# Kernel optimization log

Measured on AMD Instinct MI355X. Metric: run time of the kernel, lower is better.

Reference implementation:

```python
import jax, jax.numpy as jnp
import numpy as np

B, S, T = 32, 64, 64
D = 512          # model_size == controller hidden == cell_size
R = 4            # read heads
M = 64           # nr_cells
V = 10000        # vocab
IF = R * D + 3 * D + 5 * R + 3   # DNC interface vector size (3607)
NN_IN = D + R * D                # controller input: x + read vectors
CLIP = 20.0
EPS = 1e-6


def _cosine(mem, keys):
    # mem (B,m,w), keys (B,h,w) -> (B,h,m) batched cosine similarity
    mn = mem / (jnp.linalg.norm(mem, axis=2, keepdims=True) + EPS)
    kn = keys / (jnp.linalg.norm(keys, axis=2, keepdims=True) + EPS)
    return jnp.einsum('bhw,bmw->bhm', kn, mn)


def _allocate(usage):
    # usage (B,m) -> allocation weights (B,1,m)
    u = EPS + (1.0 - EPS) * usage
    phi = jnp.argsort(u, axis=1)                      # ascending: least used first
    su = jnp.take_along_axis(u, phi, axis=1)
    excl = jnp.cumprod(jnp.concatenate([jnp.ones_like(su[:, :1]), su[:, :-1]], axis=1), axis=1)
    sa = (1.0 - su) * excl
    return jnp.take_along_axis(sa, jnp.argsort(phi, axis=1), axis=1)[:, None, :]


def _memory_step(xi, st):
    memory, link, prec, rw, ww, usage = st
    b = xi.shape[0]
    # --- parse interface vector (same slicing as dnc.Memory, independent_linears=False) ---
    rk = jnp.tanh(xi[:, :R * D].reshape(b, R, D))                        # read keys
    rs = jax.nn.softplus(xi[:, R * D:R * D + R])                         # read strengths
    wk = jnp.tanh(xi[:, R * D + R:R * D + R + D].reshape(b, 1, D))       # write key
    ws = jax.nn.softplus(xi[:, R * D + R + D])[:, None]                  # write strength
    er = jax.nn.sigmoid(xi[:, R * D + R + D + 1:R * D + R + 2 * D + 1].reshape(b, 1, D))
    wv = jnp.tanh(xi[:, R * D + R + 2 * D + 1:R * D + R + 3 * D + 1].reshape(b, 1, D))
    fg = jax.nn.sigmoid(xi[:, R * D + R + 3 * D + 1:R * D + 2 * R + 3 * D + 1])   # free gates
    ag = jax.nn.sigmoid(xi[:, R * D + 2 * R + 3 * D + 1])[:, None, None]          # alloc gate
    wg = jax.nn.sigmoid(xi[:, R * D + 2 * R + 3 * D + 2])[:, None, None]          # write gate
    modes = jax.nn.softmax(xi[:, R * D + 2 * R + 3 * D + 3:R * D + 5 * R + 3 * D + 3].reshape(b, R, 3), axis=2)
    # --- write ---
    usage = usage + (1 - usage) * (1 - jnp.prod(1 - ww, axis=1))
    usage = usage * jnp.prod(1 - fg[:, :, None] * rw, axis=1)
    wcw = jax.nn.softmax(_cosine(memory, wk) * ws[:, :, None], axis=2)   # (B,1,M)
    alloc = _allocate(usage)
    ww = wg * (ag * alloc + (1 - ag) * wcw)                              # (B,1,M)
    reset = jnp.prod(1 - ww[:, :, :, None] * er[:, :, None, :], axis=1)  # (B,M,D)
    memory = memory * reset + jnp.einsum('bhm,bhw->bmw', ww, wv)
    ww_i, ww_j = ww[:, :, :, None], ww[:, :, None, :]
    link = (1 - ww_i - ww_j) * link + ww_i * prec[:, :, None, :]
    link = link * (1 - jnp.eye(M, dtype=link.dtype))                     # zero diagonal
    prec = (1 - jnp.sum(ww, axis=2, keepdims=True)) * prec + ww
    # --- read ---
    cw = jax.nn.softmax(_cosine(memory, rk) * rs[:, :, None], axis=2)    # (B,R,M)
    l0 = link[:, 0]
    fwd = jnp.einsum('bnm,brm->brn', l0, rw)
    bwd = jnp.einsum('bmn,brm->brn', l0, rw)
    rw = modes[:, :, 0:1] * bwd + modes[:, :, 1:2] * fwd + modes[:, :, 2:3] * cw
    rv = jnp.einsum('brm,bmw->brw', rw, memory)                          # read vectors
    return (memory, link, prec, rw, ww, usage), rv


def _lstm_cell(x, h, c, Wih, Whh, bih, bhh):
    g = x @ Wih.T + bih + h @ Whh.T + bhh
    i, f, gg, o = jnp.split(g, 4, axis=-1)
    c2 = jax.nn.sigmoid(f) * c + jax.nn.sigmoid(i) * jnp.tanh(gg)
    return jax.nn.sigmoid(o) * jnp.tanh(c2), c2


def _dnc_run(x, p, mem0):
    # x: (B,L,D). Faithful to ixaxaar dnc.py: each timestep input is concat(x_t, initial last_read=zeros).
    b, L, _ = x.shape
    xin = jnp.concatenate([x, jnp.zeros((b, L, R * D), x.dtype)], axis=-1)
    h = jnp.zeros((2, b, D), x.dtype)
    c = jnp.zeros((2, b, D), x.dtype)

    def step(carry, x_t):
        (h, c), mem = carry
        h0, c0 = _lstm_cell(x_t, h[0], c[0], p['Wih0'], p['Whh0'], p['bih0'], p['bhh0'])
        h1, c1 = _lstm_cell(h0, h[1], c[1], p['Wih1'], p['Whh1'], p['bih1'], p['bhh1'])
        out = jnp.clip(h1, -CLIP, CLIP)
        xi = out @ p['Wi'].T + p['bi']
        mem, rv = _memory_step(xi, mem)
        full = jnp.concatenate([out, rv.reshape(b, R * D)], axis=-1)
        y = full @ p['Wo'].T + p['bo']
        return ((jnp.stack([h0, h1]), jnp.stack([c0, c1])), mem), y

    (_, memT), ys = jax.lax.scan(step, ((h, c), mem0), jnp.swapaxes(xin, 0, 1))
    return jnp.swapaxes(ys, 0, 1), memT


def _init_mem(b, dtype):
    return (jnp.zeros((b, M, D), dtype), jnp.zeros((b, 1, M, M), dtype),
            jnp.zeros((b, 1, M), dtype), jnp.zeros((b, R, M), dtype),
            jnp.zeros((b, 1, M), dtype), jnp.zeros((b, M), dtype))


_PNAMES = ['Wih0', 'Whh0', 'bih0', 'bhh0', 'Wih1', 'Whh1', 'bih1', 'bhh1', 'Wi', 'bi', 'Wo', 'bo']


def setup_inputs() -> dict:
    key = jax.random.key(0)
    ks = iter(jax.random.split(key, 40))

    def p(shape, s=0.05):
        return jax.random.normal(next(ks), shape, dtype=jnp.float32) * s

    d = {'emb_src': p((V, D), 0.5), 'emb_tgt': p((V, D), 0.5)}
    shapes = [(4 * D, NN_IN), (4 * D, D), (4 * D,), (4 * D,), (4 * D, D), (4 * D, D), (4 * D,), (4 * D,),
              (IF, D), (IF,), (D, NN_IN), (D,)]
    for pre in ('enc', 'dec'):
        for n, sh in zip(_PNAMES, shapes):
            d[pre + '_' + n] = p(sh)
    d['fc_W'] = p((V, D))
    d['fc_b'] = p((V,))
    d['input'] = jax.random.randint(next(ks), (B, S), 0, V, dtype=jnp.int32)
    d['tgt'] = jax.random.randint(next(ks), (B, T), 0, V, dtype=jnp.int32)
    return d


def reference(emb_src, emb_tgt,
              enc_Wih0, enc_Whh0, enc_bih0, enc_bhh0, enc_Wih1, enc_Whh1, enc_bih1, enc_bhh1,
              enc_Wi, enc_bi, enc_Wo, enc_bo,
              dec_Wih0, dec_Whh0, dec_bih0, dec_bhh0, dec_Wih1, dec_Whh1, dec_bih1, dec_bhh1,
              dec_Wi, dec_bi, dec_Wo, dec_bo,
              fc_W, fc_b, input, tgt):
    enc_vals = [enc_Wih0, enc_Whh0, enc_bih0, enc_bhh0, enc_Wih1, enc_Whh1, enc_bih1, enc_bhh1,
                enc_Wi, enc_bi, enc_Wo, enc_bo]
    dec_vals = [dec_Wih0, dec_Whh0, dec_bih0, dec_bhh0, dec_Wih1, dec_Whh1, dec_bih1, dec_bhh1,
                dec_Wi, dec_bi, dec_Wo, dec_bo]
    enc_p = dict(zip(_PNAMES, enc_vals))
    dec_p = dict(zip(_PNAMES, dec_vals))
    src = emb_src[input]                                   # (B,S,D)
    _, mem = _dnc_run(src, enc_p, _init_mem(src.shape[0], src.dtype))
    out, _ = _dnc_run(emb_tgt[tgt], dec_p, mem)            # decoder reuses encoder memory state
    logits = out @ fc_W.T + fc_b                           # (B,T,V)
    return jnp.transpose(logits, (0, 2, 1))                # (B,V,T)
```

## Files before the change

### kernel.cpp

```cpp
#include <hip/hip_runtime.h>

#define BB   32
#define DD   512
#define RR   4
#define MM   64
#define VV   10000
#define TT   64
#define IFX  3607
#define NNIN 2560
#define EPSF 1e-6f

typedef unsigned short u16;

__device__ __forceinline__ float bf(u16 u){ return __uint_as_float(((unsigned)u)<<16); }
__device__ __forceinline__ float4 b4f(ushort4 u){
  float4 f; f.x = bf(u.x); f.y = bf(u.y); f.z = bf(u.z); f.w = bf(u.w); return f;
}
__device__ __forceinline__ u16 f2b(float f){
  unsigned u = __float_as_uint(f);
  u += 0x7fffu + ((u>>16)&1u);
  return (u16)(u>>16);
}
__device__ __forceinline__ float sigmf(float x){ return 1.f/(1.f+__expf(-x)); }
__device__ __forceinline__ float softplusf(float x){ return x > 20.f ? x : log1pf(__expf(x)); }
__device__ __forceinline__ float wredSum(float v){
  #pragma unroll
  for (int s=1;s<64;s<<=1) v += __shfl_xor(v,s,64);
  return v;
}
__device__ __forceinline__ float wredMax(float v){
  #pragma unroll
  for (int s=1;s<64;s<<=1) v = fmaxf(v, __shfl_xor(v,s,64));
  return v;
}

__device__ __forceinline__ float ldg_c(const float* p){
  return __hip_atomic_load(const_cast<float*>(p), __ATOMIC_RELAXED, __HIP_MEMORY_SCOPE_AGENT);
}
__device__ __forceinline__ void stg_c(float* p, float v){
  __hip_atomic_store(p, v, __ATOMIC_RELAXED, __HIP_MEMORY_SCOPE_AGENT);
}
__device__ __forceinline__ unsigned ldg_cu(const unsigned* p){
  return __hip_atomic_load(const_cast<unsigned*>(p), __ATOMIC_RELAXED, __HIP_MEMORY_SCOPE_AGENT);
}
__device__ __forceinline__ void stg_cu(unsigned* p, unsigned v){
  __hip_atomic_store(p, v, __ATOMIC_RELAXED, __HIP_MEMORY_SCOPE_AGENT);
}

__device__ __forceinline__ void ldg_cv4x2(const float* p0,const float* p1, float4& a,float4& b){
  asm volatile("global_load_dwordx4 %0, %2, off sc0 sc1\n\t"
               "global_load_dwordx4 %1, %3, off sc0 sc1\n\t"
               "s_waitcnt vmcnt(0)"
               : "=&v"(a),"=&v"(b)
               : "v"(p0),"v"(p1)
               : "memory");
}
__device__ __forceinline__ void ldg_c4s(const float* p0,const float* p1,const float* p2,const float* p3,
                                        float& a,float& b,float& c,float& d){
  asm volatile("global_load_dword %0, %4, off sc0 sc1\n\t"
               "global_load_dword %1, %5, off sc0 sc1\n\t"
               "global_load_dword %2, %6, off sc0 sc1\n\t"
               "global_load_dword %3, %7, off sc0 sc1\n\t"
               "s_waitcnt vmcnt(0)"
               : "=&v"(a),"=&v"(b),"=&v"(c),"=&v"(d)
               : "v"(p0),"v"(p1),"v"(p2),"v"(p3)
               : "memory");
}
__device__ __forceinline__ void ldg_c2s(const float* p0,const float* p1, float& a,float& b){
  asm volatile("global_load_dword %0, %2, off sc0 sc1\n\t"
               "global_load_dword %1, %3, off sc0 sc1\n\t"
               "s_waitcnt vmcnt(0)"
               : "=&v"(a),"=&v"(b)
               : "v"(p0),"v"(p1)
               : "memory");
}

#define SM_FLOATS 9600
#define NBLK 256u
#define NTHR 512

__device__ __forceinline__ void gbar5(unsigned* flags, unsigned* gen, unsigned ep){
  asm volatile("s_waitcnt vmcnt(0) lgkmcnt(0)" ::: "memory");
  __syncthreads();
  if (threadIdx.x == 0) stg_cu(&flags[blockIdx.x*16], ep);
  if (blockIdx.x == 0) {
    if (threadIdx.x < 256) {
      const unsigned* f = &flags[threadIdx.x*16];
      while (ldg_cu(f) < ep) __builtin_amdgcn_s_sleep(1);
    }
    __syncthreads();
    if (threadIdx.x == 0) stg_cu(gen, ep);
  } else if (threadIdx.x == 0) {
    while (ldg_cu(gen) < ep) __builtin_amdgcn_s_sleep(1);
  }
  __syncthreads();
}

#define LW_OFF 5312
#define XW_OFF 4224

__device__ __forceinline__ void preload_lstm(float* S, int tile,
    const float* __restrict__ Wx, int wx_stride, const float* __restrict__ Wh)
{
  float* WL = S + LW_OFF;
  const int tid = threadIdx.x;
  const int dblk = tile*8;
  for (int i = tid; i < 8192; i += NTHR) {
    const int r  = i >> 8;
    const int k4 = (i & 255) * 4;
    const int gr = ((r>>3)<<9) + dblk + (r&7);
    float4 v;
    if (k4 < 512) v = *(const float4*)&Wx[(size_t)gr*wx_stride + k4];
    else          v = *(const float4*)&Wh[(size_t)gr*512 + (k4-512)];
    *(float4*)&WL[r*1028 + k4] = v;
  }
}

__device__ __forceinline__ void preload_xi(float* S, int xtile, const float* __restrict__ Wi){
  float* XW = S + XW_OFF;
  const int tid = threadIdx.x;
  for (int i = tid; i < 8192; i += NTHR) {
    const int r  = i >> 7;
    const int k4 = (i & 127) * 4;
    int cr = xtile*64 + r; if (cr >= IFX) cr = IFX-1;
    *(float4*)&XW[r*516 + k4] = *(const float4*)&Wi[(size_t)cr*512 + k4];
  }
}

__device__ __noinline__ void lstm_tile_p(
    float* S, int tile,
    const float* __restrict__ bx, const float* __restrict__ bh,
    const float* emb, const int* seq, int t,
    const float* xf,
    const float* hprev, float* hcur,
    float* cst, float* outc, u16* full)
{
  float (*As)[132] = (float(*)[132])S;
  int* idxs = (int*)(S + 5280);
  const float* WL = S + LW_OFF;
  const int tid = threadIdx.x;
  const int w  = tid >> 6;
  const int bg = (tid >> 3) & 7;
  const int ks = tid & 7;
  const int dblk = tile * 8;
  const int ba = tid >> 5;
  const int bbs = ba + 16;
  const int f0 = (tid & 31) * 4;
  float acc[4][4];
  #pragma unroll
  for (int i=0;i<4;i++)
    #pragma unroll
    for (int j=0;j<4;j++) acc[i][j]=0.f;
  if (emb != nullptr && tid < 32) idxs[tid] = seq[tid*64 + t];
  __syncthreads();
  #define LSRC(ch, bb_) ( ((ch) < 4) \
      ? ((emb != nullptr) ? &emb[(size_t)idxs[bb_]*512 + (ch)*128 + f0] \
                          : &xf[(bb_)*512 + (ch)*128 + f0]) \
      : &hprev[(bb_)*512 + ((ch)*128 - 512) + f0] )
  for (int chunk = 0; chunk < 8; ++chunk) {
    {
      float4 v0, v1;
      ldg_cv4x2(LSRC(chunk,ba), LSRC(chunk,bbs), v0, v1);
      *(float4*)&As[ba][f0]  = v0;
      *(float4*)&As[bbs][f0] = v1;
    }
    __syncthreads();
    const int kb = chunk*128;
    #pragma unroll
    for (int m = 0; m < 4; ++m) {
      const int kk = ks*4 + m*32;
      float4 w4[4], a4[4];
      #pragma unroll
      for (int j=0;j<4;j++) w4[j] = *(const float4*)&WL[(w + 8*j)*1028 + kb + kk];
      #pragma unroll
      for (int i=0;i<4;i++) a4[i] = *(const float4*)&As[bg + 8*i][kk];
      #pragma unroll
      for (int i=0;i<4;i++)
        #pragma unroll
        for (int j=0;j<4;j++)
          acc[i][j] = fmaf(a4[i].x,w4[j].x, fmaf(a4[i].y,w4[j].y,
                      fmaf(a4[i].z,w4[j].z, fmaf(a4[i].w,w4[j].w, acc[i][j]))));
    }
    __syncthreads();
  }
  #undef LSRC
  #pragma unroll
  for (int i=0;i<4;i++)
    #pragma unroll
    for (int j=0;j<4;j++){
      float v = acc[i][j];
      v += __shfl_xor(v,1,64);
      v += __shfl_xor(v,2,64);
      v += __shfl_xor(v,4,64);
      acc[i][j] = v;
    }
  if (ks == 0) {
    const int d = dblk + w;
    float bias[4];
    #pragma unroll
    for (int j=0;j<4;j++){
      const int gcol = (j<<9) + d;
      bias[j] = bx[gcol] + bh[gcol];
    }
    #pragma unroll
    for (int i=0;i<4;i++){
      const int b = bg + 8*i;
      const int cid = b*512 + d;
      const float gi = acc[i][0] + bias[0];
      const float gf = acc[i][1] + bias[1];
      const float gg = acc[i][2] + bias[2];
      const float go = acc[i][3] + bias[3];
      const float cv = sigmf(gf)*cst[cid] + sigmf(gi)*tanhf(gg);
      const float hv = sigmf(go)*tanhf(cv);
      cst[cid] = cv;
      stg_c(&hcur[cid], hv);
      if (outc != nullptr) {
        const float oc = fminf(fmaxf(hv,-20.f),20.f);
        stg_c(&outc[cid], oc);
        if (full != nullptr) full[((size_t)t*32 + b)*2560 + d] = f2b(oc);
      }
    }
  }
  __syncthreads();
}

__device__ __noinline__ void xi_tile_p(
    float* S, int xtile,
    const float* outc, const float* __restrict__ bi, float* xi)
{
  float (*As)[132] = (float(*)[132])S;
  const float* XW = S + XW_OFF;
  const int tid = threadIdx.x;
  const int w  = tid >> 6;
  const int l  = tid & 63;
  const int tt = l >> 2;
  const int ks = l & 3;
  const int cg = 2*w + (tt>>3);
  const int bg = tt & 7;
  const int ba = tid >> 5;
  const int bbs = ba + 16;
  const int f0 = (tid & 31) * 4;
  float acc[4][4];
  #pragma unroll
  for (int i=0;i<4;i++)
    #pragma unroll
    for (int j=0;j<4;j++) acc[i][j]=0.f;
  for (int chunk = 0; chunk < 4; ++chunk) {
    {
      const int kb0 = chunk*128;
      float4 v0, v1;
      ldg_cv4x2(&outc[ba*512 + kb0 + f0], &outc[bbs*512 + kb0 + f0], v0, v1);
      *(float4*)&As[ba][f0]  = v0;
      *(float4*)&As[bbs][f0] = v1;
    }
    __syncthreads();
    const int kb = chunk*128;
    #pragma unroll
    for (int m = 0; m < 8; ++m) {
      const int kk = ks*4 + m*16;
      float4 w4[4], a4[4];
      #pragma unroll
      for (int j=0;j<4;j++) w4[j] = *(const float4*)&XW[(cg + 16*j)*516 + kb + kk];
      #pragma unroll
      for (int i=0;i<4;i++) a4[i] = *(const float4*)&As[bg + 8*i][kk];
      #pragma unroll
      for (int i=0;i<4;i++)
        #pragma unroll
        for (int j=0;j<4;j++)
          acc[i][j] = fmaf(a4[i].x,w4[j].x, fmaf(a4[i].y,w4[j].y,
                      fmaf(a4[i].z,w4[j].z, fmaf(a4[i].w,w4[j].w, acc[i][j]))));
    }
    __syncthreads();
  }
  #pragma unroll
  for (int i=0;i<4;i++)
    #pragma unroll
    for (int j=0;j<4;j++){
      float v = acc[i][j];
      v += __shfl_xor(v,1,64);
      v += __shfl_xor(v,2,64);
      acc[i][j] = v;
    }
  if (ks == 0) {
    #pragma unroll
    for (int j=0;j<4;j++){
      const int col = xtile*64 + cg + 16*j;
      if (col < IFX) {
        const float bias = bi[col];
        #pragma unroll
        for (int i=0;i<4;i++)
          stg_c(&xi[(size_t)(bg + 8*i)*IFX + col], acc[i][j] + bias);
      }
    }
  }
  __syncthreads();
}

__device__ __constant__ int kSidx[23] = {
  2048,2049,2050,2051, 2564, 3589,3590,3591,3592, 3593, 3594,
  3595,3596,3597, 3598,3599,3600, 3601,3602,3603, 3604,3605,3606
};

#define MEMPITCH 516
#define L_MEM   0
#define L_LINK  33024
#define L_RK    37184
#define L_WK    39232
#define L_RWP   39744
#define L_PREC  40000
#define L_USAGE 40064
#define L_WCW   40128
#define L_U     40192
#define L_WW    40256
#define L_CWA   40320
#define L_SC    40576
#define L_SRAW  40616
#define L_END   40640
#define DYN_LDS_BYTES 162560

__device__ __noinline__ void mem_tile_lds(
    float* S, int b, const float* xi, u16* full, int t)
{
  const int tid = threadIdx.x;
  const float* xb = xi + (size_t)b*IFX;
  float* MEMS = S + L_MEM;
  float* LNK  = S + L_LINK;
  float (*rk_s)[512] = (float(*)[512])(S + L_RK);
  float* wk_s  = S + L_WK;
  float* RWP   = S + L_RWP;
  float* PREC  = S + L_PREC;
  float* USAGE = S + L_USAGE;
  float* wcw_s = S + L_WCW;
  float* u_s   = S + L_U;
  float* WW    = S + L_WW;
  float* sorted_s = S + L_CWA;
  float* excl_s   = S + L_CWA + 64;
  int*   rank_s   = (int*)(S + L_CWA + 128);
  float (*cw_s)[64] = (float(*)[64])(S + L_CWA);
  float* sc   = S + L_SC;
  float* sraw = S + L_SRAW;

  {
    const float* base = xb + tid*4;
    float v0,v1,v2,v3;
    ldg_c4s(base+0,base+1,base+2,base+3, v0,v1,v2,v3);
    float* d = &rk_s[tid>>7][(tid&127)*4];
    d[0]=tanhf(v0); d[1]=tanhf(v1); d[2]=tanhf(v2); d[3]=tanhf(v3);
  }
  if (tid < 128) {
    const float* base = xb + 2052 + tid*4;
    float v0,v1,v2,v3;
    ldg_c4s(base+0,base+1,base+2,base+3, v0,v1,v2,v3);
    float* d = &wk_s[tid*4];
    d[0]=tanhf(v0); d[1]=tanhf(v1); d[2]=tanhf(v2); d[3]=tanhf(v3);
  }
  if (tid < 23) sraw[tid] = ldg_c(&xb[kSidx[tid]]);
  __syncthreads();
  if (tid == 0) {
    for (int r=0;r<4;r++) sc[r] = softplusf(sraw[r]);
    sc[4] = softplusf(sraw[4]);
    for (int r=0;r<4;r++) sc[5+r] = sigmf(sraw[5+r]);
    sc[9]  = sigmf(sraw[9]);
    sc[10] = sigmf(sraw[10]);
    for (int r=0;r<4;r++) {
      const float a0=sraw[11+3*r], a1=sraw[12+3*r], a2=sraw[13+3*r];
      const float mx=fmaxf(a0,fmaxf(a1,a2));
      const float e0=__expf(a0-mx), e1=__expf(a1-mx), e2=__expf(a2-mx);
      const float s=e0+e1+e2;
      sc[11+3*r]=e0/s; sc[12+3*r]=e1/s; sc[13+3*r]=e2/s;
    }
  }
  if (tid < 256) {
    const int wid = tid>>6, ln = tid&63;
    float p = 0.f;
    for (int i = ln; i < 512; i += 64) { const float v = rk_s[wid][i]; p = fmaf(v,v,p); }
    p = wredSum(p);
    if (ln == 0) sc[24+wid] = sqrtf(p);
    if (wid == 1) {
      float q2 = 0.f;
      for (int i = ln; i < 512; i += 64) { const float v = wk_s[i]; q2 = fmaf(v,v,q2); }
      q2 = wredSum(q2);
      if (ln == 0) sc[23] = sqrtf(q2);
    }
  }
  __syncthreads();
  if (tid < 256) {
    const int m = tid>>2, q = tid&3;
    const float* mr = MEMS + m*MEMPITCH;
    float d = 0.f, ss = 0.f;
    for (int i = q*128; i < q*128+128; i += 4) {
      const float4 mv = *(const float4*)&mr[i];
      d = fmaf(mv.x, wk_s[i  ], d); d = fmaf(mv.y, wk_s[i+1], d);
      d = fmaf(mv.z, wk_s[i+2], d); d = fmaf(mv.w, wk_s[i+3], d);
      ss = fmaf(mv.x,mv.x,ss); ss = fmaf(mv.y,mv.y,ss);
      ss = fmaf(mv.z,mv.z,ss); ss = fmaf(mv.w,mv.w,ss);
    }
    d  += __shfl_xor(d,1,64);  d  += __shfl_xor(d,2,64);
    ss += __shfl_xor(ss,1,64); ss += __shfl_xor(ss,2,64);
    if (q == 0) wcw_s[m] = d / ((sqrtf(ss)+EPSF)*(sc[23]+EPSF)) * sc[4];
  }
  if (tid < 64) {
    const float uo = USAGE[tid];
    float u = uo + (1.f-uo)*WW[tid];
    #pragma unroll
    for (int r=0;r<4;r++) u *= (1.f - sc[5+r]*RWP[r*64+tid]);
    USAGE[tid] = u;
  }
  __syncthreads();
  if (tid < 64) {
    const float v = wcw_s[tid];
    const float mx = wredMax(v);
    const float e = __expf(v-mx);
    const float s2 = wredSum(e);
    wcw_s[tid] = e/s2;
    u_s[tid] = EPSF + (1.f-EPSF)*USAGE[tid];
  }
  __syncthreads();
  if (tid < 64) {
    const float u = u_s[tid]; int rk2 = 0;
    for (int j=0;j<64;j++){ const float uj = u_s[j]; rk2 += (uj<u) || (uj==u && j<tid); }
    rank_s[tid] = rk2; sorted_s[rk2] = u;
  }
  __syncthreads();
  if (tid == 0) { float run = 1.f; for (int p2=0;p2<64;p2++){ excl_s[p2]=run; run*=sorted_s[p2]; } }
  __syncthreads();
  if (tid < 64) {
    const float al = (1.f - u_s[tid]) * excl_s[rank_s[tid]];
    const float wwv = sc[10]*(sc[9]*al + (1.f-sc[9])*wcw_s[tid]);
    WW[tid] = wwv;
    const float s3 = wredSum(wwv);
    if (tid==0) sc[28] = s3;
  }
  __syncthreads();
  {
    float e0,w0;
    ldg_c2s(&xb[2565+tid], &xb[3077+tid], e0, w0);
    const float er0 = sigmf(e0);
    const float wv0 = tanhf(w0);
    #pragma unroll 4
    for (int m=0;m<64;m++){
      const float wwm = WW[m];
      float* p = MEMS + m*MEMPITCH + tid;
      p[0] = p[0]*(1.f - wwm*er0) + wwm*wv0;
    }
  }
  __syncthreads();
  for (int e = tid; e < 4096; e += NTHR) {
    const int i2 = e>>6, j2 = e&63;
    const float lv = LNK[i2*65+j2];
    LNK[i2*65+j2] = (i2==j2) ? 0.f
               : ((1.f - WW[i2] - WW[j2])*lv + WW[i2]*PREC[j2]);
  }
  __syncthreads();
  if (tid < 64) PREC[tid] = (1.f - sc[28])*PREC[tid] + WW[tid];
  __syncthreads();
  const int r6 = tid>>6, m6 = tid&63;
  if (tid < 256) {
    const float* mr = MEMS + m6*MEMPITCH;
    const float* rkr = rk_s[r6];
    float d = 0.f, ss = 0.f;
    for (int i=0;i<512;i+=4){
      const float4 mv = *(const float4*)&mr[i];
      d = fmaf(mv.x, rkr[i  ], d); d = fmaf(mv.y, rkr[i+1], d);
      d = fmaf(mv.z, rkr[i+2], d); d = fmaf(mv.w, rkr[i+3], d);
      ss = fmaf(mv.x,mv.x,ss); ss = fmaf(mv.y,mv.y,ss);
      ss = fmaf(mv.z,mv.z,ss); ss = fmaf(mv.w,mv.w,ss);
    }
    const float cv = d / ((sqrtf(ss)+EPSF)*(sc[24+r6]+EPSF)) * sc[r6];
    const float mx = wredMax(cv);
    const float e = __expf(cv-mx);
    const float s2 = wredSum(e);
    cw_s[r6][m6] = e/s2;
  }
  __syncthreads();
  float rn = 0.f;
  if (tid < 256) {
    float fw = 0.f, bw = 0.f;
    #pragma unroll 8
    for (int m3=0;m3<64;m3++){
      const float rp = RWP[r6*64+m3];
      fw = fmaf(LNK[m6*65+m3], rp, fw);
      bw = fmaf(LNK[m3*65+m6], rp, bw);
    }
    rn = sc[11+3*r6]*bw + sc[12+3*r6]*fw + sc[13+3*r6]*cw_s[r6][m6];
  }
  __syncthreads();
  if (tid < 256) RWP[r6*64+m6] = rn;
  __syncthreads();
  if (full != nullptr && tid < 256) {
    const int l = tid&63, r8 = tid>>6;
    float a[8];
    #pragma unroll
    for (int j=0;j<8;j++) a[j]=0.f;
    for (int m3=0;m3<64;m3++){
      const float rv_ = RWP[r8*64+m3];
      const float* mr = MEMS + m3*MEMPITCH + 2*l;
      #pragma unroll
      for (int j=0;j<4;j++){
        const float2 v = *(const float2*)&mr[128*j];
        a[2*j]   = fmaf(rv_, v.x, a[2*j]);
        a[2*j+1] = fmaf(rv_, v.y, a[2*j+1]);
      }
    }
    u16* dst = full + ((size_t)t*32 + b)*2560 + 512 + r8*512;
    #pragma unroll
    for (int j=0;j<4;j++){
      const unsigned wd = (unsigned)f2b(a[2*j]) | ((unsigned)f2b(a[2*j+1])<<16);
      *(unsigned*)&dst[2*l + 128*j] = wd;
    }
  }
  __syncthreads();
}

__device__ __noinline__ void lstm_tile_g(
    float* sm, int tile,
    const float* __restrict__ Wx, int wx_stride,
    const float* __restrict__ Wh,
    const float* __restrict__ bx, const float* __restrict__ bh,
    const float* emb, const int* seq, int t,
    const float* xf,
    const float* hprev, float* hcur,
    float* cst, float* outc, u16* full)
{
  float (*As)[132] = (float(*)[132])sm;
  float (*Ws)[132] = (float(*)[132])(sm + 4224);
  float* gs = sm + 8448;
  int* idxs = (int*)(sm + 9504);
  const int tid = threadIdx.x;
  const int c = tid & 31;
  const int dblk = tile * 8;
  const int gcol = ((c>>3)<<9) + dblk + (c&7);
  const int b0 = (tid >> 5) * 4;
  float acc0=0.f, acc1=0.f, acc2=0.f, acc3=0.f;
  if (emb != nullptr && tid < 32) idxs[tid] = seq[tid*64 + t];
  __syncthreads();
  for (int chunk = 0; chunk < 8; ++chunk) {
    const int k0 = chunk * 128;
    const bool xp = (chunk < 4);
    for (int i = tid; i < 1024; i += 256) {
      const int bb2 = i >> 5, f4i = (i & 31)*4;
      if (xp && emb != nullptr) {
        *(float4*)&As[bb2][f4i] = *(const float4*)&emb[(size_t)idxs[bb2]*512 + k0 + f4i];
      } else {
        const float* src = xp ? &xf[bb2*512 + k0 + f4i]
                              : &hprev[bb2*512 + (k0-512) + f4i];
        As[bb2][f4i+0] = ldg_c(src+0);
        As[bb2][f4i+1] = ldg_c(src+1);
        As[bb2][f4i+2] = ldg_c(src+2);
        As[bb2][f4i+3] = ldg_c(src+3);
      }
    }
    for (int i = tid; i < 1024; i += 256) {
      const int r = i >> 5, f4i = (i & 31)*4;
      const int gr = ((r>>3)<<9) + dblk + (r&7);
      const float4 v = xp ? *(const float4*)&Wx[(size_t)gr*wx_stride + k0 + f4i]
                          : *(const float4*)&Wh[(size_t)gr*512 + (k0-512) + f4i];
      *(float4*)&Ws[r][f4i] = v;
    }
    __syncthreads();
    #pragma unroll 8
    for (int kk = 0; kk < 128; kk += 4) {
      const float4 w4 = *(const float4*)&Ws[c][kk];
      const float4 a0 = *(const float4*)&As[b0+0][kk];
      const float4 a1 = *(const float4*)&As[b0+1][kk];
      const float4 a2 = *(const float4*)&As[b0+2][kk];
      const float4 a3 = *(const float4*)&As[b0+3][kk];
      acc0 = fmaf(a0.x,w4.x,fmaf(a0.y,w4.y,fmaf(a0.z,w4.z,fmaf(a0.w,w4.w,acc0))));
      acc1 = fmaf(a1.x,w4.x,fmaf(a1.y,w4.y,fmaf(a1.z,w4.z,fmaf(a1.w,w4.w,acc1))));
      acc2 = fmaf(a2.x,w4.x,fmaf(a2.y,w4.y,fmaf(a2.z,w4.z,fmaf(a2.w,w4.w,acc2))));
      acc3 = fmaf(a3.x,w4.x,fmaf(a3.y,w4.y,fmaf(a3.z,w4.z,fmaf(a3.w,w4.w,acc3))));
    }
    __syncthreads();
  }
  const float bias = bx[gcol] + bh[gcol];
  gs[c*33 + b0+0] = acc0 + bias;
  gs[c*33 + b0+1] = acc1 + bias;
  gs[c*33 + b0+2] = acc2 + bias;
  gs[c*33 + b0+3] = acc3 + bias;
  __syncthreads();
  {
    const int b2 = tid & 31, dl2 = tid >> 5;
    const float gi = gs[(0*8+dl2)*33 + b2];
    const float gf = gs[(1*8+dl2)*33 + b2];
    const float gg = gs[(2*8+dl2)*33 + b2];
    const float go = gs[(3*8+dl2)*33 + b2];
    const int d = dblk + dl2;
    const int cid = b2*512 + d;
    const float cv = sigmf(gf)*cst[cid] + sigmf(gi)*tanhf(gg);
    const float hv = sigmf(go)*tanhf(cv);
    cst[cid] = cv;
    stg_c(&hcur[cid], hv);
    if (outc != nullptr) {
      const float oc = fminf(fmaxf(hv,-20.f),20.f);
      stg_c(&outc[cid], oc);
      if (full != nullptr) full[((size_t)t*32 + b2)*2560 + d] = f2b(oc);
    }
  }
  __syncthreads();
}

__device__ __noinline__ void xi_tile_g(
    float* sm, int tile,
    const float* outc,
    const float* __restrict__ Wi, const float* __restrict__ bi,
    float* xi)
{
  float (*As)[132] = (float(*)[132])sm;
  float (*Ws)[132] = (float(*)[132])(sm + 4224);
  const int tid = threadIdx.x;
  const int c = tid & 31;
  const int col = tile*32 + c;
  const int b0 = (tid>>5)*4;
  float acc0=0.f,acc1=0.f,acc2=0.f,acc3=0.f;
  for (int chunk = 0; chunk < 4; ++chunk) {
    const int k0 = chunk*128;
    for (int i = tid; i < 1024; i += 256) {
      const int bb2 = i>>5, f4i = (i&31)*4;
      const float* src = &outc[bb2*512 + k0 + f4i];
      As[bb2][f4i+0] = ldg_c(src+0);
      As[bb2][f4i+1] = ldg_c(src+1);
      As[bb2][f4i+2] = ldg_c(src+2);
      As[bb2][f4i+3] = ldg_c(src+3);
    }
    for (int i = tid; i < 1024; i += 256) {
      const int r = i>>5, f4i = (i&31)*4;
      int cr = tile*32 + r; cr = cr < IFX ? cr : IFX-1;
      *(float4*)&Ws[r][f4i] = *(const float4*)&Wi[(size_t)cr*512 + k0 + f4i];
    }
    __syncthreads();
    #pragma unroll 8
    for (int kk = 0; kk < 128; kk += 4) {
      const float4 w4 = *(const float4*)&Ws[c][kk];
      const float4 a0 = *(const float4*)&As[b0+0][kk];
      const float4 a1 = *(const float4*)&As[b0+1][kk];
      const float4 a2 = *(const float4*)&As[b0+2][kk];
      const float4 a3 = *(const float4*)&As[b0+3][kk];
      acc0 = fmaf(a0.x,w4.x,fmaf(a0.y,w4.y,fmaf(a0.z,w4.z,fmaf(a0.w,w4.w,acc0))));
      acc1 = fmaf(a1.x,w4.x,fmaf(a1.y,w4.y,fmaf(a1.z,w4.z,fmaf(a1.w,w4.w,acc1))));
      acc2 = fmaf(a2.x,w4.x,fmaf(a2.y,w4.y,fmaf(a2.z,w4.z,fmaf(a2.w,w4.w,acc2))));
      acc3 = fmaf(a3.x,w4.x,fmaf(a3.y,w4.y,fmaf(a3.z,w4.z,fmaf(a3.w,w4.w,acc3))));
    }
    __syncthreads();
  }
  if (col < IFX) {
    const float bias = bi[col];
    stg_c(&xi[(size_t)(b0+0)*IFX + col], acc0 + bias);
    stg_c(&xi[(size_t)(b0+1)*IFX + col], acc1 + bias);
    stg_c(&xi[(size_t)(b0+2)*IFX + col], acc2 + bias);
    stg_c(&xi[(size_t)(b0+3)*IFX + col], acc3 + bias);
  }
  __syncthreads();
}

__device__ __noinline__ void mem_tile_g(
    float* sm, int b,
    const float* xi,
    float* mem,
    float* link, float* prec,
    float* rwg, float* wwg, float* usg,
    u16* full, int t)
{
  const int tid = threadIdx.x;
  const float* xb = xi + (size_t)b*IFX;
  float (*rk_s)[512]  = (float(*)[512])sm;
  float* wk_s   = sm + 2048;
  float* er_s   = sm + 2560;
  float* wv_s   = sm + 3072;
  float (*rwp_s)[64]  = (float(*)[64])(sm + 3584);
  float* prec_s = sm + 3840;
  float* usage_s= sm + 3904;
  float* wcw_s  = sm + 3968;
  float* u_s    = sm + 4032;
  float* ww_s   = sm + 4096;
  float* sorted_s = sm + 4160;
  float* excl_s = sm + 4224;
  int*   rank_s = (int*)(sm + 4288);
  float (*cw_s)[64]  = (float(*)[64])(sm + 4352);
  float (*rwn_s)[64] = (float(*)[64])(sm + 4608);
  float* mn_s   = sm + 4864;
  float* sc     = sm + 4928;
  float (*link_s)[65] = (float(*)[65])(sm + 4976);

  for (int i = tid; i < 2048; i += 256) rk_s[i>>9][i&511] = tanhf(ldg_c(&xb[i]));
  for (int i = tid; i < 512; i += 256) {
    wk_s[i] = tanhf(ldg_c(&xb[2052+i]));
    er_s[i] = sigmf(ldg_c(&xb[2565+i]));
    wv_s[i] = tanhf(ldg_c(&xb[3077+i]));
  }
  rwp_s[tid>>6][tid&63] = rwg[b*256 + tid];
  if (tid < 64) { prec_s[tid] = prec[b*64+tid]; usage_s[tid] = usg[b*64+tid]; }
  if (tid == 0) {
    for (int r=0;r<4;r++) sc[r] = softplusf(ldg_c(&xb[2048+r]));
    sc[4] = softplusf(ldg_c(&xb[2564]));
    for (int r=0;r<4;r++) sc[5+r] = sigmf(ldg_c(&xb[3589+r]));
    sc[9]  = sigmf(ldg_c(&xb[3593]));
    sc[10] = sigmf(ldg_c(&xb[3594]));
    for (int r=0;r<4;r++) {
      const float a0=ldg_c(&xb[3595+3*r]), a1=ldg_c(&xb[3596+3*r]), a2=ldg_c(&xb[3597+3*r]);
      const float mx=fmaxf(a0,fmaxf(a1,a2));
      const float e0=__expf(a0-mx), e1=__expf(a1-mx), e2=__expf(a2-mx);
      const float s=e0+e1+e2;
      sc[11+3*r]=e0/s; sc[12+3*r]=e1/s; sc[13+3*r]=e2/s;
    }
  }
  __syncthreads();
  {
    const int wid = tid>>6, ln = tid&63;
    float p = 0.f;
    for (int i = ln; i < 512; i += 64) { const float v = rk_s[wid][i]; p = fmaf(v,v,p); }
    p = wredSum(p);
    if (ln == 0) sc[24+wid] = sqrtf(p);
    if (wid == 1) {
      float q2 = 0.f;
      for (int i = ln; i < 512; i += 64) { const float v = wk_s[i]; q2 = fmaf(v,v,q2); }
      q2 = wredSum(q2);
      if (ln == 0) sc[23] = sqrtf(q2);
    }
  }
  __syncthreads();
  {
    const int m = tid>>2, q = tid&3;
    const float* mr = mem + ((size_t)b*64 + m)*512;
    float d = 0.f, ss = 0.f;
    for (int i = q*128; i < q*128+128; i += 4) {
      const float4 mv = *(const float4*)&mr[i];
      d = fmaf(mv.x, wk_s[i  ], d); d = fmaf(mv.y, wk_s[i+1], d);
      d = fmaf(mv.z, wk_s[i+2], d); d = fmaf(mv.w, wk_s[i+3], d);
      ss = fmaf(mv.x,mv.x,ss); ss = fmaf(mv.y,mv.y,ss);
      ss = fmaf(mv.z,mv.z,ss); ss = fmaf(mv.w,mv.w,ss);
    }
    d  += __shfl_xor(d,1,64);  d  += __shfl_xor(d,2,64);
    ss += __shfl_xor(ss,1,64); ss += __shfl_xor(ss,2,64);
    if (q == 0) wcw_s[m] = d / ((sqrtf(ss)+EPSF)*(sc[23]+EPSF)) * sc[4];
  }
  if (tid < 64) {
    const float uo = usage_s[tid];
    const float wwp = wwg[b*64+tid];
    float u = uo + (1.f-uo)*wwp;
    #pragma unroll
    for (int r=0;r<4;r++) u *= (1.f - sc[5+r]*rwp_s[r][tid]);
    usage_s[tid] = u; usg[b*64+tid] = u;
  }
  __syncthreads();
  if (tid < 64) {
    const float v = wcw_s[tid];
    const float mx = wredMax(v);
    const float e = __expf(v-mx);
    const float s2 = wredSum(e);
    wcw_s[tid] = e/s2;
    u_s[tid] = EPSF + (1.f-EPSF)*usage_s[tid];
  }
  __syncthreads();
  if (tid < 64) {
    const float u = u_s[tid]; int rk2 = 0;
    for (int j=0;j<64;j++){ const float uj = u_s[j]; rk2 += (uj<u) || (uj==u && j<tid); }
    rank_s[tid] = rk2; sorted_s[rk2] = u;
  }
  __syncthreads();
  if (tid == 0) { float run = 1.f; for (int p2=0;p2<64;p2++){ excl_s[p2]=run; run*=sorted_s[p2]; } }
  __syncthreads();
  if (tid < 64) {
    const float al = (1.f - u_s[tid]) * excl_s[rank_s[tid]];
    const float wwv = sc[10]*(sc[9]*al + (1.f-sc[9])*wcw_s[tid]);
    ww_s[tid] = wwv; wwg[b*64+tid] = wwv;
    const float s3 = wredSum(wwv);
    if (tid==0) sc[28] = s3;
  }
  __syncthreads();
  {
    const int m = tid>>2, q = tid&3;
    const float wwm = ww_s[m];
    float* mr = mem + ((size_t)b*64 + m)*512;
    float ss = 0.f;
    for (int i = q*128; i < q*128+128; i += 4) {
      float4 mv = *(const float4*)&mr[i];
      mv.x = mv.x*(1.f - wwm*er_s[i  ]) + wwm*wv_s[i  ];
      mv.y = mv.y*(1.f - wwm*er_s[i+1]) + wwm*wv_s[i+1];
      mv.z = mv.z*(1.f - wwm*er_s[i+2]) + wwm*wv_s[i+2];
      mv.w = mv.w*(1.f - wwm*er_s[i+3]) + wwm*wv_s[i+3];
      *(float4*)&mr[i] = mv;
      ss += mv.x*mv.x + mv.y*mv.y + mv.z*mv.z + mv.w*mv.w;
    }
    ss += __shfl_xor(ss,1,64); ss += __shfl_xor(ss,2,64);
    if (q==0) mn_s[m] = sqrtf(ss);
  }
  __syncthreads();
  {
    float* lrow = link + (size_t)b*4096;
    for (int e = tid; e < 4096; e += 256) {
      const int i2 = e>>6, j2 = e&63;
      const float ln2 = (i2==j2) ? 0.f
                 : ((1.f - ww_s[i2] - ww_s[j2])*lrow[e] + ww_s[i2]*prec_s[j2]);
      link_s[i2][j2] = ln2;
      lrow[e] = ln2;
    }
  }
  if (tid < 64) prec[b*64+tid] = (1.f - sc[28])*prec_s[tid] + ww_s[tid];
  __syncthreads();
  const int r6 = tid>>6, m6 = tid&63;
  {
    const float* mr = mem + ((size_t)b*64 + m6)*512;
    const float* rkr = rk_s[r6];
    float d = 0.f;
    for (int i=0;i<512;i+=4){
      const float4 mv = *(const float4*)&mr[i];
      d = fmaf(mv.x, rkr[i  ], d); d = fmaf(mv.y, rkr[i+1], d);
      d = fmaf(mv.z, rkr[i+2], d); d = fmaf(mv.w, rkr[i+3], d);
    }
    const float cv = d / ((mn_s[m6]+EPSF)*(sc[24+r6]+EPSF)) * sc[r6];
    const float mx = wredMax(cv);
    const float e = __expf(cv-mx);
    const float s2 = wredSum(e);
    cw_s[r6][m6] = e/s2;
  }
  __syncthreads();
  {
    float fw = 0.f, bw = 0.f;
    #pragma unroll 8
    for (int m3=0;m3<64;m3++){
      const float rp = rwp_s[r6][m3];
      fw = fmaf(link_s[m6][m3], rp, fw);
      bw = fmaf(link_s[m3][m6], rp, bw);
    }
    const float rn = sc[11+3*r6]*bw + sc[12+3*r6]*fw + sc[13+3*r6]*cw_s[r6][m6];
    rwn_s[r6][m6] = rn;
    rwg[b*256 + r6*64 + m6] = rn;
  }
  __syncthreads();
  if (full != nullptr) {
    const int r8 = tid>>6, w0 = (tid&63)*8;
    float a[8];
    #pragma unroll
    for (int j=0;j<8;j++) a[j]=0.f;
    for (int m3=0;m3<64;m3++){
      const float rv_ = rwn_s[r8][m3];
      const float* mr = mem + ((size_t)b*64+m3)*512 + w0;
      const float4 p0 = *(const float4*)&mr[0];
      const float4 p1 = *(const float4*)&mr[4];
      a[0]=fmaf(rv_,p0.x,a[0]); a[1]=fmaf(rv_,p0.y,a[1]);
      a[2]=fmaf(rv_,p0.z,a[2]); a[3]=fmaf(rv_,p0.w,a[3]);
      a[4]=fmaf(rv_,p1.x,a[4]); a[5]=fmaf(rv_,p1.y,a[5]);
      a[6]=fmaf(rv_,p1.z,a[6]); a[7]=fmaf(rv_,p1.w,a[7]);
    }
    u16* dst = full + ((size_t)t*32 + b)*2560 + 512 + r8*512 + w0;
    ushort4 s0, s1;
    s0.x=f2b(a[0]); s0.y=f2b(a[1]); s0.z=f2b(a[2]); s0.w=f2b(a[3]);
    s1.x=f2b(a[4]); s1.y=f2b(a[5]); s1.z=f2b(a[6]); s1.w=f2b(a[7]);
    *(ushort4*)dst = s0;
    *(ushort4*)(dst+4) = s1;
  }
  __syncthreads();
}

struct StepArgs {
  const float* emb[2];
  const int*   seq[2];
  const float* Wx0[2]; const float* Wh0[2]; const float* bx0[2]; const float* bh0[2];
  const float* Wx1[2]; const float* Wh1[2]; const float* bx1[2]; const float* bh1[2];
  const float* Wi[2];  const float* bi[2];
  float* h0[2]; float* h1[2]; float* c0; float* c1;
  float* xi2[2]; float* oc[2];
  u16* full;
  unsigned* flags; unsigned* gen;
};

__global__ __launch_bounds__(NTHR) void k_all(StepArgs a) {
  extern __shared__ float S[];
  const int bid = blockIdx.x;
  const int role = (bid < 64) ? 0 : (bid < 128) ? 1 : (bid < 185) ? 2 : (bid < 217) ? 3 : 4;
  unsigned ep = 0;
  if (role == 3) {
    for (int i = threadIdx.x; i < L_END; i += NTHR) S[i] = 0.f;
  }
  __syncthreads();
  for (int ph = 0; ph < 2; ++ph) {
    if (role == 0)      preload_lstm(S, bid,    a.Wx0[ph], NNIN, a.Wh0[ph]);
    else if (role == 1) preload_lstm(S, bid-64, a.Wx1[ph], 512,  a.Wh1[ph]);
    else if (role == 2) preload_xi(S, bid-128, a.Wi[ph]);
    for (int i = bid*NTHR + threadIdx.x; i < 16384; i += (int)(NBLK*NTHR)) {
      stg_c(&a.h0[0][i],0.f); stg_c(&a.h0[1][i],0.f);
      stg_c(&a.h1[0][i],0.f); stg_c(&a.h1[1][i],0.f);
    }
    if (role == 0 && threadIdx.x < 256) {
      const int cid = (threadIdx.x & 31)*512 + bid*8 + (threadIdx.x >> 5);
      a.c0[cid] = 0.f;
    } else if (role == 1 && threadIdx.x < 256) {
      const int cid = (threadIdx.x & 31)*512 + (bid-64)*8 + (threadIdx.x >> 5);
      a.c1[cid] = 0.f;
    }
    gbar5(a.flags, a.gen, ++ep);
    u16* fullp = ph ? a.full : nullptr;
    for (int k = 0; k <= TT+2; ++k) {
      float* h0r = a.h0[(k+1)&1];
      float* h0w = a.h0[k&1];
      float* h1r = a.h1[k&1];
      float* h1w = a.h1[(k+1)&1];
      float* ocw = a.oc[(k+1)&1];
      float* ocr = a.oc[k&1];
      float* xiw = a.xi2[k&1];
      float* xir = a.xi2[(k+1)&1];
      if (role == 0) {
        if (k < TT)
          lstm_tile_p(S, bid, a.bx0[ph], a.bh0[ph], a.emb[ph], a.seq[ph], k,
                      nullptr, h0r, h0w, a.c0, nullptr, nullptr);
      } else if (role == 1) {
        if (k >= 1 && k <= TT)
          lstm_tile_p(S, bid-64, a.bx1[ph], a.bh1[ph], nullptr, nullptr, k-1,
                      h0r, h1r, h1w, a.c1, ocw, fullp);
      } else if (role == 2) {
        if (k >= 2 && k <= TT+1)
          xi_tile_p(S, bid-128, ocr, a.bi[ph], xiw);
      } else if (role == 3) {
        if (k >= 3)
          mem_tile_lds(S, bid-185, xir, fullp, k-3);
      }
      gbar5(a.flags, a.gen, ++ep);
    }
  }
}

__global__ __launch_bounds__(256) void k_lstm(
    const float* Wx, int wx_stride, const float* Wh,
    const float* bx, const float* bh,
    const float* emb, const int* seq, int t, const float* xf,
    const float* hprev, float* hcur, float* cst, float* outc, u16* full)
{
  __shared__ __align__(16) float sm[SM_FLOATS];
  lstm_tile_g(sm, blockIdx.x, Wx, wx_stride, Wh, bx, bh, emb, seq, t, xf,
              hprev, hcur, cst, outc, full);
}
__global__ __launch_bounds__(256) void k_xi(
    const float* outc, const float* Wi, const float* bi, float* xi)
{
  __shared__ __align__(16) float sm[SM_FLOATS];
  xi_tile_g(sm, blockIdx.x, outc, Wi, bi, xi);
}
__global__ __launch_bounds__(256) void k_mem(
    const float* xi, float* mem, float* link, float* prec,
    float* rwg, float* wwg, float* usg, u16* full, int t)
{
  __shared__ __align__(16) float sm[SM_FLOATS];
  mem_tile_g(sm, blockIdx.x, xi, mem, link, prec, rwg, wwg, usg, full, t);
}

__global__ __launch_bounds__(256) void k_y(
    const u16* __restrict__ full,
    const float* __restrict__ Wo, const float* __restrict__ bo,
    u16* __restrict__ y)
{
  __shared__ __align__(16) float As[32][136];
  const int tid = threadIdx.x;
  const int rb = blockIdx.x >> 4, cb = blockIdx.x & 15;
  const int c = tid & 31, col = cb*32 + c;
  const int b0 = (tid>>5)*4;
  float acc0=0.f,acc1=0.f,acc2=0.f,acc3=0.f;
  for (int chunk = 0; chunk < 20; ++chunk) {
    const int k0 = chunk*128;
    for (int i = tid; i < 1024; i += 256) {
      const int r = i>>5, kk = (i&31)*4;
      const float4 v = b4f(*(const ushort4*)&full[(size_t)(rb*32+r)*2560 + k0 + kk]);
      *(float4*)&As[r][kk] = v;
    }
    __syncthreads();
    const float* Wr = Wo + (size_t)col*2560 + k0;
    #pragma unroll 8
    for (int kk = 0; kk < 128; kk += 4) {
      const float4 w4 = *(const float4*)(Wr + kk);
      const float4 a0 = *(const float4*)&As[b0+0][kk];
      const float4 a1 = *(const float4*)&As[b0+1][kk];
      const float4 a2 = *(const float4*)&As[b0+2][kk];
      const float4 a3 = *(const float4*)&As[b0+3][kk];
      acc0 = fmaf(a0.x,w4.x,fmaf(a0.y,w4.y,fmaf(a0.z,w4.z,fmaf(a0.w,w4.w,acc0))));
      acc1 = fmaf(a1.x,w4.x,fmaf(a1.y,w4.y,fmaf(a1.z,w4.z,fmaf(a1.w,w4.w,acc1))));
      acc2 = fmaf(a2.x,w4.x,fmaf(a2.y,w4.y,fmaf(a2.z,w4.z,fmaf(a2.w,w4.w,acc2))));
      acc3 = fmaf(a3.x,w4.x,fmaf(a3.y,w4.y,fmaf(a3.z,w4.z,fmaf(a3.w,w4.w,acc3))));
    }
    __syncthreads();
  }
  const float bias = bo[col];
  y[(size_t)(rb*32+b0+0)*512+col] = f2b(acc0+bias);
  y[(size_t)(rb*32+b0+1)*512+col] = f2b(acc1+bias);
  y[(size_t)(rb*32+b0+2)*512+col] = f2b(acc2+bias);
  y[(size_t)(rb*32+b0+3)*512+col] = f2b(acc3+bias);
}

__global__ __launch_bounds__(256) void k_logits(
    const u16* __restrict__ y,
    const float* __restrict__ fcW, const float* __restrict__ fcb,
    float* __restrict__ outp)
{
  __shared__ __align__(16) float As[64][68];
  const int tid = threadIdx.x;
  const int bb = blockIdx.x / 157, vt = blockIdx.x % 157;
  const int tl = tid & 15, vl = tid >> 4;
  const int t0 = tl*4;
  const int vbase = vt*64 + vl*4;
  float acc[4][4];
  #pragma unroll
  for (int i=0;i<4;i++)
    #pragma unroll
    for (int j=0;j<4;j++) acc[i][j]=0.f;
  for (int chunk = 0; chunk < 8; ++chunk) {
    const int k0 = chunk*64;
    for (int i = tid; i < 1024; i += 256) {
      const int tt = i>>4, kk = (i&15)*4;
      const float4 v = b4f(*(const ushort4*)&y[((size_t)tt*32 + bb)*512 + k0 + kk]);
      *(float4*)&As[tt][kk] = v;
    }
    __syncthreads();
    for (int kk = 0; kk < 64; kk += 4) {
      const float4 a0 = *(const float4*)&As[t0+0][kk];
      const float4 a1 = *(const float4*)&As[t0+1][kk];
      const float4 a2 = *(const float4*)&As[t0+2][kk];
      const float4 a3 = *(const float4*)&As[t0+3][kk];
      #pragma unroll
      for (int vj = 0; vj < 4; ++vj) {
        const int v = vbase + vj;
        const int vc = v < VV ? v : VV-1;
        const float4 w4 = *(const float4*)(fcW + (size_t)vc*512 + k0 + kk);
        acc[vj][0] = fmaf(a0.x,w4.x,fmaf(a0.y,w4.y,fmaf(a0.z,w4.z,fmaf(a0.w,w4.w,acc[vj][0]))));
        acc[vj][1] = fmaf(a1.x,w4.x,fmaf(a1.y,w4.y,fmaf(a1.z,w4.z,fmaf(a1.w,w4.w,acc[vj][1]))));
        acc[vj][2] = fmaf(a2.x,w4.x,fmaf(a2.y,w4.y,fmaf(a2.z,w4.z,fmaf(a2.w,w4.w,acc[vj][2]))));
        acc[vj][3] = fmaf(a3.x,w4.x,fmaf(a3.y,w4.y,fmaf(a3.z,w4.z,fmaf(a3.w,w4.w,acc[vj][3]))));
      }
    }
    __syncthreads();
  }
  #pragma unroll
  for (int vj = 0; vj < 4; ++vj) {
    const int v = vbase + vj;
    if (v < VV) {
      const float bias = fcb[v];
      float4 st;
      st.x = acc[vj][0]+bias;
      st.y = acc[vj][1]+bias;
      st.z = acc[vj][2]+bias;
      st.w = acc[vj][3]+bias;
      *(float4*)&outp[(size_t)bb*640000 + (size_t)v*64 + t0] = st;
    }
  }
}

#define O_H0A 0
#define O_H0B 16384
#define O_H1A 32768
#define O_H1B 49152
#define O_C0  65536
#define O_C1  81920
#define O_MEM 98304
#define O_FLAGS 98304
#define O_XI2   102400
#define O_OC2   217824
#define O_LINK  1146880
#define O_PREC  1277952
#define O_RW    1280000
#define O_WW    1288192
#define O_USAGE 1290240
#define STATE_FLOATS 1292288
#define O_BAR  1292288
#define O_XI   1292544
#define O_OUT  1407968
#define F32_END 1424352
#define FULL_BYTE_OFF 5697408ull
#define Y_BYTE_OFF    16183168ull
#define WS_NEED       18280320ull

extern "C" void kernel_launch(void* const* d_in, const int* in_sizes, int n_in,
                              void* d_out, int out_size, void* d_ws, size_t ws_size,
                              hipStream_t stream) {
  (void)in_sizes; (void)n_in; (void)out_size;
  if (ws_size < WS_NEED) return;
  typedef const float* cf;
  cf emb_src = (cf)d_in[0], emb_tgt = (cf)d_in[1];
  cf eW[12], dWt[12];
  for (int i=0;i<12;i++){ eW[i]=(cf)d_in[2+i]; dWt[i]=(cf)d_in[14+i]; }
  cf fcW = (cf)d_in[26], fcb = (cf)d_in[27];
  const int* inp = (const int*)d_in[28];
  const int* tgt = (const int*)d_in[29];
  float* outp = (float*)d_out;
  float* w = (float*)d_ws;

  float* h0buf[2] = { w+O_H0A, w+O_H0B };
  float* h1buf[2] = { w+O_H1A, w+O_H1B };
  float* c0 = w+O_C0;  float* c1 = w+O_C1;
  float* memb = w+O_MEM;
  float* linkb = w+O_LINK; float* precb = w+O_PREC;
  float* rwb = w+O_RW;     float* wwb = w+O_WW;   float* usageb = w+O_USAGE;
  float* xib = w+O_XI;     float* outb = w+O_OUT;
  u16* fullb = (u16*)((char*)d_ws + FULL_BYTE_OFF);
  u16* yb    = (u16*)((char*)d_ws + Y_BYTE_OFF);

  hipMemsetAsync(w, 0, (size_t)(STATE_FLOATS+256)*4, stream);

  StepArgs sa;
  sa.emb[0]=emb_src; sa.emb[1]=emb_tgt;
  sa.seq[0]=inp;     sa.seq[1]=tgt;
  sa.Wx0[0]=eW[0]; sa.Wh0[0]=eW[1]; sa.bx0[0]=eW[2]; sa.bh0[0]=eW[3];
  sa.Wx1[0]=eW[4]; sa.Wh1[0]=eW[5]; sa.bx1[0]=eW[6]; sa.bh1[0]=eW[7];
  sa.Wi[0]=eW[8];  sa.bi[0]=eW[9];
  sa.Wx0[1]=dWt[0]; sa.Wh0[1]=dWt[1]; sa.bx0[1]=dWt[2]; sa.bh0[1]=dWt[3];
  sa.Wx1[1]=dWt[4]; sa.Wh1[1]=dWt[5]; sa.bx1[1]=dWt[6]; sa.bh1[1]=dWt[7];
  sa.Wi[1]=dWt[8];  sa.bi[1]=dWt[9];
  sa.h0[0]=h0buf[0]; sa.h0[1]=h0buf[1];
  sa.h1[0]=h1buf[0]; sa.h1[1]=h1buf[1];
  sa.c0=c0; sa.c1=c1;
  sa.xi2[0]=xib;      sa.xi2[1]=w+O_XI2;
  sa.oc[0]=outb;      sa.oc[1]=w+O_OC2;
  sa.full=fullb;
  sa.flags=(unsigned*)(w + O_FLAGS);
  sa.gen=(unsigned*)(w + O_BAR);

  (void)hipFuncSetAttribute((const void*)k_all,
      hipFuncAttributeMaxDynamicSharedMemorySize, DYN_LDS_BYTES);

  void* kargs[] = { &sa };
  hipError_t err = hipLaunchCooperativeKernel((const void*)k_all, dim3(NBLK), dim3(NTHR),
                                              kargs, DYN_LDS_BYTES, stream);
  if (err != hipSuccess) {
    int pp = 0;
    for (int t = 0; t < TT; ++t) {
      k_lstm<<<64,256,0,stream>>>(eW[0], NNIN, eW[1], eW[2], eW[3],
                                  emb_src, inp, t, nullptr,
                                  h0buf[pp], h0buf[pp^1], c0, nullptr, nullptr);
      k_lstm<<<64,256,0,stream>>>(eW[4], 512, eW[5], eW[6], eW[7],
                                  nullptr, nullptr, t, h0buf[pp^1],
                                  h1buf[pp], h1buf[pp^1], c1, outb, nullptr);
      k_xi<<<113,256,0,stream>>>(outb, eW[8], eW[9], xib);
      k_mem<<<32,256,0,stream>>>(xib, memb, linkb, precb, rwb, wwb, usageb,
                                 nullptr, t);
      pp ^= 1;
    }
    hipMemsetAsync(w, 0, (size_t)O_MEM*4, stream);
    pp = 0;
    for (int t = 0; t < TT; ++t) {
      k_lstm<<<64,256,0,stream>>>(dWt[0], NNIN, dWt[1], dWt[2], dWt[3],
                                  emb_tgt, tgt, t, nullptr,
                                  h0buf[pp], h0buf[pp^1], c0, nullptr, nullptr);
      k_lstm<<<64,256,0,stream>>>(dWt[4], 512, dWt[5], dWt[6], dWt[7],
                                  nullptr, nullptr, t, h0buf[pp^1],
                                  h1buf[pp], h1buf[pp^1], c1, outb, fullb);
      k_xi<<<113,256,0,stream>>>(outb, dWt[8], dWt[9], xib);
      k_mem<<<32,256,0,stream>>>(xib, memb, linkb, precb, rwb, wwb, usageb,
                                 fullb, t);
      pp ^= 1;
    }
  }

  k_y<<<1024,256,0,stream>>>(fullb, dWt[10], dWt[11], yb);
  k_logits<<<32*157,256,0,stream>>>(yb, fcW, fcb, outp);
}
```

Measured before the change: 4.249 ms.

## Use flat all-to-all grid barrier, relax load cache bits, parallelize exclusive cumprod

Replaces the two-level grid barrier, in which block 0 gathers all flags and then publishes a generation word, with a flat barrier where every block polls all 256 flags directly. This removes one serialized round-trip per step. Coherent loads drop the sc0 bit and keep only sc1, which changes the cache scope of those loads. The serial 64-element exclusive cumulative product in the allocation step becomes a wavefront shuffle scan. The flat barrier adds heavy polling traffic from every block, and the cache-bit change could weaken coherence.

After: 4.100 ms. -3.5%, faster.

```diff
diff --git a/kernel.cpp b/kernel.cpp
--- a/kernel.cpp
+++ b/kernel.cpp
@@ -48,8 +48,8 @@
 }
 
 __device__ __forceinline__ void ldg_cv4x2(const float* p0,const float* p1, float4& a,float4& b){
-  asm volatile("global_load_dwordx4 %0, %2, off sc0 sc1\n\t"
-               "global_load_dwordx4 %1, %3, off sc0 sc1\n\t"
+  asm volatile("global_load_dwordx4 %0, %2, off sc1\n\t"
+               "global_load_dwordx4 %1, %3, off sc1\n\t"
                "s_waitcnt vmcnt(0)"
                : "=&v"(a),"=&v"(b)
                : "v"(p0),"v"(p1)
@@ -57,18 +57,18 @@
 }
 __device__ __forceinline__ void ldg_c4s(const float* p0,const float* p1,const float* p2,const float* p3,
                                         float& a,float& b,float& c,float& d){
-  asm volatile("global_load_dword %0, %4, off sc0 sc1\n\t"
-               "global_load_dword %1, %5, off sc0 sc1\n\t"
-               "global_load_dword %2, %6, off sc0 sc1\n\t"
-               "global_load_dword %3, %7, off sc0 sc1\n\t"
+  asm volatile("global_load_dword %0, %4, off sc1\n\t"
+               "global_load_dword %1, %5, off sc1\n\t"
+               "global_load_dword %2, %6, off sc1\n\t"
+               "global_load_dword %3, %7, off sc1\n\t"
                "s_waitcnt vmcnt(0)"
                : "=&v"(a),"=&v"(b),"=&v"(c),"=&v"(d)
                : "v"(p0),"v"(p1),"v"(p2),"v"(p3)
                : "memory");
 }
 __device__ __forceinline__ void ldg_c2s(const float* p0,const float* p1, float& a,float& b){
-  asm volatile("global_load_dword %0, %2, off sc0 sc1\n\t"
-               "global_load_dword %1, %3, off sc0 sc1\n\t"
+  asm volatile("global_load_dword %0, %2, off sc1\n\t"
+               "global_load_dword %1, %3, off sc1\n\t"
                "s_waitcnt vmcnt(0)"
                : "=&v"(a),"=&v"(b)
                : "v"(p0),"v"(p1)
@@ -79,19 +79,13 @@
 #define NBLK 256u
 #define NTHR 512
 
-__device__ __forceinline__ void gbar5(unsigned* flags, unsigned* gen, unsigned ep){
+__device__ __forceinline__ void gbar6(unsigned* flags, unsigned ep){
   asm volatile("s_waitcnt vmcnt(0) lgkmcnt(0)" ::: "memory");
   __syncthreads();
   if (threadIdx.x == 0) stg_cu(&flags[blockIdx.x*16], ep);
-  if (blockIdx.x == 0) {
-    if (threadIdx.x < 256) {
-      const unsigned* f = &flags[threadIdx.x*16];
-      while (ldg_cu(f) < ep) __builtin_amdgcn_s_sleep(1);
-    }
-    __syncthreads();
-    if (threadIdx.x == 0) stg_cu(gen, ep);
-  } else if (threadIdx.x == 0) {
-    while (ldg_cu(gen) < ep) __builtin_amdgcn_s_sleep(1);
+  if (threadIdx.x < 256) {
+    const unsigned* f = &flags[threadIdx.x*16];
+    while (ldg_cu(f) < ep) __builtin_amdgcn_s_sleep(1);
   }
   __syncthreads();
 }
@@ -422,7 +416,18 @@
     rank_s[tid] = rk2; sorted_s[rk2] = u;
   }
   __syncthreads();
-  if (tid == 0) { float run = 1.f; for (int p2=0;p2<64;p2++){ excl_s[p2]=run; run*=sorted_s[p2]; } }
+  if (tid < 64) {
+    float v = sorted_s[tid];
+    float inc = v;
+    #pragma unroll
+    for (int s=1;s<64;s<<=1){
+      const float tshf = __shfl_up(inc, s, 64);
+      if (tid >= s) inc *= tshf;
+    }
+    float exc = __shfl_up(inc, 1, 64);
+    if (tid == 0) exc = 1.f;
+    excl_s[tid] = exc;
+  }
   __syncthreads();
   if (tid < 64) {
     const float al = (1.f - u_s[tid]) * excl_s[rank_s[tid]];
@@ -888,7 +893,7 @@
       const int cid = (threadIdx.x & 31)*512 + (bid-64)*8 + (threadIdx.x >> 5);
       a.c1[cid] = 0.f;
     }
-    gbar5(a.flags, a.gen, ++ep);
+    gbar6(a.flags, ++ep);
     u16* fullp = ph ? a.full : nullptr;
     for (int k = 0; k <= TT+2; ++k) {
       float* h0r = a.h0[(k+1)&1];
@@ -914,7 +919,7 @@
         if (k >= 3)
           mem_tile_lds(S, bid-185, xir, fullp, k-3);
       }
-      gbar5(a.flags, a.gen, ++ep);
+      gbar6(a.flags, ++ep);
     }
   }
 }
```
